# Kernel tuning notes

Measured on AMD Instinct MI355X. Metric: run time of the kernel, lower is better.

## Reference

```python
import jax, jax.numpy as jnp
import numpy as np

G = 7          # gauss_order
Q = G * G      # quadrature points
B1, B2 = 2048, 256
LOG2PI = float(np.log(2.0 * np.pi))


def _quadrature(g):
    # interval (-1,1) x (-1,1): halfwidth=1, mean=0
    eta, w = np.polynomial.legendre.leggauss(g)
    pts = np.stack(np.meshgrid(eta, eta, indexing='ij'), axis=0).reshape(2, -1)  # [2, G^2]
    wts = (w * w[:, None]).ravel()  # [G^2]
    return pts.astype(np.float32), wts.astype(np.float32)


def setup_inputs() -> dict:
    key = jax.random.key(0)
    k1, k2, k3, k4 = jax.random.split(key, 4)
    pts, wts = _quadrature(G)
    tv_means = jax.random.normal(k1, (B1, B2, 2), dtype=jnp.float32)
    # SPD covariances: A @ A^T + eps*I
    A = 0.5 * jax.random.normal(k2, (B1, B2, 2, 2), dtype=jnp.float32)
    tv_covars = A @ jnp.swapaxes(A, -1, -2) + 0.1 * jnp.eye(2, dtype=jnp.float32)
    # proper rotation matrices from random angles
    theta = jax.random.uniform(k3, (B1, B2), dtype=jnp.float32, minval=0.0, maxval=2.0 * np.pi)
    c, s = jnp.cos(theta), jnp.sin(theta)
    rotations = jnp.stack([jnp.stack([c, -s], -1), jnp.stack([s, c], -1)], -2)  # [B1,B2,2,2]
    translations = jax.random.normal(k4, (B1, B2, 2), dtype=jnp.float32)
    return {
        'tv_means': tv_means,
        'tv_covars': tv_covars,
        'rotations': rotations,
        'translations': translations,
        'eta_01': jnp.asarray(pts),
        'weights': jnp.asarray(wts),
    }


def reference(tv_means, tv_covars, rotations, translations, eta_01, weights):
    # gauss_pts: rotate quadrature points, then translate -> [B1,B2,Q,2]
    gauss_pts = jnp.einsum('...ij,jq->...qi', rotations, eta_01) + translations[..., None, :]
    # MVN(tv_means, tv_covars) log_prob, broadcast over quadrature dim.
    diff = gauss_pts - tv_means[..., None, :]               # [B1,B2,Q,2]
    dx, dy = diff[..., 0], diff[..., 1]                      # [B1,B2,Q]
    c00 = tv_covars[..., 0, 0][..., None]
    c01 = tv_covars[..., 0, 1][..., None]
    c10 = tv_covars[..., 1, 0][..., None]
    c11 = tv_covars[..., 1, 1][..., None]
    det = c00 * c11 - c01 * c10                              # [B1,B2,1]
    # Mahalanobis term via closed-form 2x2 inverse
    quad = (c11 * dx * dx - (c01 + c10) * dx * dy + c00 * dy * dy) / det
    logp = -0.5 * quad - LOG2PI - 0.5 * jnp.log(det)         # [B1,B2,Q]
    integral = jnp.clip(jnp.sum(jnp.exp(logp) * weights, axis=-1), 0.0, 1.0)  # [B1,B2]
    return gauss_pts, integral
```

## Files before the change

kernel.cpp:

```cpp
#include <hip/hip_runtime.h>
#include <math.h>

#define LOG2PI_F 1.8378770664093453f

__global__ __launch_bounds__(256) void gauss2d_kernel(
    const float* __restrict__ tv_means,
    const float* __restrict__ tv_covars,
    const float* __restrict__ rotations,
    const float* __restrict__ translations,
    const float* __restrict__ eta,
    const float* __restrict__ weights,
    float* __restrict__ gauss_pts,
    float* __restrict__ integral,
    unsigned int B,
    unsigned int partB_blocks)
{
    const unsigned int Q = 49u;

    if (blockIdx.x < partB_blocks) {
        unsigned int p = blockIdx.x * 256u + threadIdx.x;
        if (p >= B) return;

        const float4 R  = ((const float4*)rotations)[p];
        const float2 tr = ((const float2*)translations)[p];
        const float2 mu = ((const float2*)tv_means)[p];
        const float4 C  = ((const float4*)tv_covars)[p];

        float det     = C.x * C.w - C.y * C.z;
        float inv_det = 1.0f / det;
        float lognorm = fmaf(-0.5f, __logf(det), -LOG2PI_F);
        float c01p10  = C.y + C.z;

        float s = 0.0f;
        #pragma unroll 7
        for (int q = 0; q < 49; ++q) {
            float ex = eta[q];
            float ey = eta[49 + q];
            float gx = fmaf(R.x, ex, fmaf(R.y, ey, tr.x));
            float gy = fmaf(R.z, ex, fmaf(R.w, ey, tr.y));
            float dx = gx - mu.x;
            float dy = gy - mu.y;
            float quad = (C.w * dx * dx - c01p10 * dx * dy + C.x * dy * dy) * inv_det;
            s += weights[q] * __expf(fmaf(-0.5f, quad, lognorm));
        }
        integral[p] = fminf(fmaxf(s, 0.0f), 1.0f);
    } else {
        unsigned int t = (blockIdx.x - partB_blocks) * 256u + threadIdx.x;
        unsigned int pair = t / Q;
        unsigned int q    = t - pair * Q;
        if (pair >= B) return;

        const float4 R  = ((const float4*)rotations)[pair];
        const float2 tr = ((const float2*)translations)[pair];
        float ex = eta[q];
        float ey = eta[49 + q];
        float gx = fmaf(R.x, ex, fmaf(R.y, ey, tr.x));
        float gy = fmaf(R.z, ex, fmaf(R.w, ey, tr.y));
        ((float2*)gauss_pts)[t] = make_float2(gx, gy);
    }
}

extern "C" void kernel_launch(void* const* d_in, const int* in_sizes, int n_in,
                              void* d_out, int out_size, void* d_ws, size_t ws_size,
                              hipStream_t stream) {
    const float* tv_means     = (const float*)d_in[0];
    const float* tv_covars    = (const float*)d_in[1];
    const float* rotations    = (const float*)d_in[2];
    const float* translations = (const float*)d_in[3];
    const float* eta          = (const float*)d_in[4];
    const float* weights      = (const float*)d_in[5];

    const unsigned int B = (unsigned int)(in_sizes[0] / 2);
    float* gauss_pts = (float*)d_out;
    float* integral  = (float*)d_out + (size_t)B * 98u;

    const unsigned int partB_blocks = (B + 255u) / 256u;
    const unsigned int partA_blocks = (unsigned int)(((size_t)B * 49u + 255u) / 256u);

    dim3 grid(partA_blocks + partB_blocks);
    dim3 block(256);
    hipLaunchKernelGGL(gauss2d_kernel, grid, block, 0, stream,
                       tv_means, tv_covars, rotations, translations,
                       eta, weights, gauss_pts, integral, B, partB_blocks);
}
```

Baseline: 250.3 us.

## Fuse gauss point and integral paths with LDS-staged coalesced stores

Replaces the two-part grid with one kernel in which each block handles 32 pairs across 8 warps, each warp covering a strided subset of the quadrature points. Gauss points are computed once, staged in LDS, and written out with coalesced float4 stores. Partial integral sums are reduced through shared memory. This removes the duplicate per-pair loads and the duplicate point computation, and makes the dominant output write contiguous. The cost is LDS pressure and a block barrier. The per-pair stride of 98 floats in LDS may also cause bank conflicts on the float2 writes.

Result: no change. 254.2 us (+1.5%).

```diff
diff --git a/kernel.cpp b/kernel.cpp
--- a/kernel.cpp
+++ b/kernel.cpp
@@ -3,7 +3,7 @@
 
 #define LOG2PI_F 1.8378770664093453f
 
-__global__ __launch_bounds__(256) void gauss2d_kernel(
+__global__ __launch_bounds__(256) void gauss2d_fused(
     const float* __restrict__ tv_means,
     const float* __restrict__ tv_covars,
     const float* __restrict__ rotations,
@@ -12,51 +12,65 @@
     const float* __restrict__ weights,
     float* __restrict__ gauss_pts,
     float* __restrict__ integral,
-    unsigned int B,
-    unsigned int partB_blocks)
+    unsigned int B)
 {
-    const unsigned int Q = 49u;
+    __shared__ float lds_pts[32 * 98];
+    __shared__ float lds_s[8][32];
 
-    if (blockIdx.x < partB_blocks) {
-        unsigned int p = blockIdx.x * 256u + threadIdx.x;
-        if (p >= B) return;
+    const unsigned int tid  = threadIdx.x;
+    const unsigned int p    = tid & 31u;
+    const unsigned int g    = tid >> 5u;
+    const unsigned int base = blockIdx.x * 32u;
+    const unsigned int pg   = base + p;
 
-        const float4 R  = ((const float4*)rotations)[p];
-        const float2 tr = ((const float2*)translations)[p];
-        const float2 mu = ((const float2*)tv_means)[p];
-        const float4 C  = ((const float4*)tv_covars)[p];
+    float s = 0.0f;
+    if (pg < B) {
+        const float4 R  = ((const float4*)rotations)[pg];
+        const float2 tr = ((const float2*)translations)[pg];
+        const float2 mu = ((const float2*)tv_means)[pg];
+        const float4 C  = ((const float4*)tv_covars)[pg];
 
-        float det     = C.x * C.w - C.y * C.z;
-        float inv_det = 1.0f / det;
-        float lognorm = fmaf(-0.5f, __logf(det), -LOG2PI_F);
-        float c01p10  = C.y + C.z;
+        const float det     = C.x * C.w - C.y * C.z;
+        const float inv_det = 1.0f / det;
+        const float lognorm = fmaf(-0.5f, __logf(det), -LOG2PI_F);
+        const float c01p10  = C.y + C.z;
 
-        float s = 0.0f;
-        #pragma unroll 7
-        for (int q = 0; q < 49; ++q) {
-            float ex = eta[q];
-            float ey = eta[49 + q];
-            float gx = fmaf(R.x, ex, fmaf(R.y, ey, tr.x));
-            float gy = fmaf(R.z, ex, fmaf(R.w, ey, tr.y));
-            float dx = gx - mu.x;
-            float dy = gy - mu.y;
-            float quad = (C.w * dx * dx - c01p10 * dx * dy + C.x * dy * dy) * inv_det;
-            s += weights[q] * __expf(fmaf(-0.5f, quad, lognorm));
+        #pragma unroll
+        for (unsigned int i = 0u; i < 7u; ++i) {
+            const unsigned int q = g + (i << 3);
+            if (q < 49u) {
+                const float ex = eta[q];
+                const float ey = eta[49u + q];
+                const float gx = fmaf(R.x, ex, fmaf(R.y, ey, tr.x));
+                const float gy = fmaf(R.z, ex, fmaf(R.w, ey, tr.y));
+                *(float2*)(&lds_pts[p * 98u + (q << 1)]) = make_float2(gx, gy);
+                const float dx = gx - mu.x;
+                const float dy = gy - mu.y;
+                const float quad =
+                    (C.w * dx * dx - c01p10 * dx * dy + C.x * dy * dy) * inv_det;
+                s += weights[q] * __expf(fmaf(-0.5f, quad, lognorm));
+            }
         }
-        integral[p] = fminf(fmaxf(s, 0.0f), 1.0f);
-    } else {
-        unsigned int t = (blockIdx.x - partB_blocks) * 256u + threadIdx.x;
-        unsigned int pair = t / Q;
-        unsigned int q    = t - pair * Q;
-        if (pair >= B) return;
+    }
+    lds_s[g][p] = s;
+    __syncthreads();
 
-        const float4 R  = ((const float4*)rotations)[pair];
-        const float2 tr = ((const float2*)translations)[pair];
-        float ex = eta[q];
-        float ey = eta[49 + q];
-        float gx = fmaf(R.x, ex, fmaf(R.y, ey, tr.x));
-        float gy = fmaf(R.z, ex, fmaf(R.w, ey, tr.y));
-        ((float2*)gauss_pts)[t] = make_float2(gx, gy);
+    const unsigned int npair = (base + 32u <= B) ? 32u : (B > base ? B - base : 0u);
+    const unsigned int nfl   = npair * 98u;
+    const unsigned int nf4   = nfl >> 2;
+    float4* __restrict__ dst = (float4*)(gauss_pts + (size_t)base * 98u);
+    const float4* __restrict__ src = (const float4*)lds_pts;
+    for (unsigned int k = tid; k < nf4; k += 256u) dst[k] = src[k];
+    if ((nfl & 3u) && tid == 0u) {
+        *(float2*)(gauss_pts + (size_t)base * 98u + (size_t)(nf4 << 2)) =
+            *(const float2*)(&lds_pts[nf4 << 2]);
+    }
+
+    if (tid < 32u && pg < B) {
+        float t = 0.0f;
+        #pragma unroll
+        for (int gg = 0; gg < 8; ++gg) t += lds_s[gg][tid];
+        integral[pg] = fminf(fmaxf(t, 0.0f), 1.0f);
     }
 }
 
@@ -74,12 +88,9 @@
     float* gauss_pts = (float*)d_out;
     float* integral  = (float*)d_out + (size_t)B * 98u;
 
-    const unsigned int partB_blocks = (B + 255u) / 256u;
-    const unsigned int partA_blocks = (unsigned int)(((size_t)B * 49u + 255u) / 256u);
-
-    dim3 grid(partA_blocks + partB_blocks);
+    dim3 grid((B + 31u) / 32u);
     dim3 block(256);
-    hipLaunchKernelGGL(gauss2d_kernel, grid, block, 0, stream,
+    hipLaunchKernelGGL(gauss2d_fused, grid, block, 0, stream,
                        tv_means, tv_covars, rotations, translations,
-                       eta, weights, gauss_pts, integral, B, partB_blocks);
+                       eta, weights, gauss_pts, integral, B);
 }
```
